# Kernel tuning notes

Hardware: AMD Instinct MI355X
Metric: run time of the kernel (lower is better)

Reference implementation:

```python
import jax, jax.numpy as jnp
import numpy as np

B, CIN, H, W = 8, 1, 192, 192
COUT, KH, KW = 8, 7, 7


def setup_inputs() -> dict:
    key = jax.random.key(0)
    k1, k2, k3 = jax.random.split(key, 3)
    x = jax.random.normal(k1, (B, CIN, H, W), dtype=jnp.float32)
    # original init: filter ~ N(0, 0.01), alpha = 0 (use small nonzero alpha)
    filt = 0.01 * jax.random.normal(k2, (COUT, CIN, KH, KW), dtype=jnp.float32)
    alpha = 0.1 * jax.random.normal(k3, (COUT, CIN), dtype=jnp.float32)
    return {"x": x, "filt": filt, "alpha": alpha}


def _smorph(x, filt, alpha):
    # x: [B, Cin, H, W]; filt: [Cout, Cin, kh, kw]; alpha: [Cout, Cin]
    b, cin, h, w = x.shape
    cout, _, kh, kw = filt.shape
    ho, wo = h - kh + 1, w - kw + 1  # 'valid' windowing as in _smorph_py
    # sliding-window patches: [B, Cin, kh*kw, Ho, Wo] (static slices, traced once)
    patches = jnp.stack(
        [x[:, :, ky:ky + ho, kx:kx + wo] for ky in range(kh) for kx in range(kw)],
        axis=2,
    )
    # s[b,co,ci,k,y,x] = input[b,ci,y+ky,x+kx] + filter[co,ci,ky,kx]
    s = patches[:, None] + filt.reshape(cout, cin, kh * kw, 1, 1)[None]
    a = alpha[None, :, :, None, None, None]  # broadcast over B, taps, space
    e = jnp.exp(a * s)
    num = jnp.sum(s * e, axis=(2, 3))  # sum over Cin and taps -> [B,Cout,Ho,Wo]
    den = jnp.sum(e, axis=(2, 3))
    return num / den


def reference(x, filt, alpha):
    # dual=False: single soft-morphology pass
    return _smorph(x, filt, alpha)
```

## Files before the change

### kernel.cpp

```cpp
#include <hip/hip_runtime.h>

#ifndef __has_builtin
#define __has_builtin(x) 0
#endif

__device__ __forceinline__ float fexp2(float v) {
#if __has_builtin(__builtin_amdgcn_exp2f)
    return __builtin_amdgcn_exp2f(v);
#else
    return exp2f(v);
#endif
}
__device__ __forceinline__ float frcp(float v) {
#if __has_builtin(__builtin_amdgcn_rcpf)
    return __builtin_amdgcn_rcpf(v);
#else
    return 1.0f / v;
#endif
}

constexpr int B_    = 8;
constexpr int H_    = 192;
constexpr int W_    = 192;
constexpr int COUT_ = 8;
constexpr int KH_   = 7;
constexpr int KW_   = 7;
constexpr int HO_   = H_ - KH_ + 1;
constexpr int WO_   = W_ - KW_ + 1;
constexpr float LOG2E = 1.44269504088896340736f;

constexpr int NTHR = 128;
constexpr int TX   = 32;
constexpr int TY   = 8;
constexpr int IX   = TX + KW_ - 1;
constexpr int IY   = TY + KH_ - 1;
constexpr int NPIX = IX * IY;
constexpr int NSLOT = (NPIX + NTHR - 1) / NTHR;

__global__ void smorph_setup(const float* __restrict__ filt,
                             const float* __restrict__ alpha,
                             float* __restrict__ ws) {
    int i = threadIdx.x;
    if (i < COUT_ * KH_) {
        int c = i / 7, ky = i - c * 7;
        float a2 = alpha[c] * LOG2E;
        float* t = ws + (c * 7 + ky) * 16;
#pragma unroll
        for (int kx = 0; kx < 7; ++kx) {
            float f = filt[(c * 7 + ky) * 7 + kx];
            float F = fexp2(a2 * f);
            t[kx]     = F;
            t[8 + kx] = F * f;
        }
        t[7] = 0.f; t[15] = 0.f;
    }
}

__global__ __launch_bounds__(NTHR, 8) void smorph_main(
    const float* __restrict__ x,
    const float* __restrict__ alpha,
    const float* __restrict__ fg,
    float* __restrict__ out)
{
    __shared__ __align__(16) float2 PH[IY * IX];

    const int tx  = threadIdx.x;
    const int ty  = threadIdx.y;
    const int tid = ty * 32 + tx;
    const int bx0 = blockIdx.x * TX;
    const int by0 = blockIdx.y * TY;
    const int z   = blockIdx.z;
    const int c   = z & 7;
    const float* xb = x + (z >> 3) * (H_ * W_);
    const float a2  = alpha[c] * LOG2E;

#pragma unroll
    for (int s = 0; s < NSLOT; ++s) {
        const int i = tid + NTHR * s;
        if (i < NPIX) {
            const int iy = i / IX, ix = i - iy * IX;
            const float xv = xb[min(by0 + iy, H_ - 1) * W_ + min(bx0 + ix, W_ - 1)];
            const float P = fexp2(a2 * xv);
            PH[i] = make_float2(P, xv * P);
        }
    }
    __syncthreads();

    const int xs = tx & 15;
    const int yr = (ty << 1) | (tx >> 4);
    const int ox = bx0 + 2 * xs;
    const int oy = by0 + yr;
    const bool vx = (ox + 1 < WO_);

    float num0 = 0.f, den0 = 0.f, num1 = 0.f, den1 = 0.f;
    const float* tc = fg + c * (7 * 16);
#pragma unroll
    for (int ky = 0; ky < KH_; ++ky) {
        const float* t = tc + ky * 16;
        const float4* rp = (const float4*)&PH[(yr + ky) * IX + 2 * xs];
        float4 q0 = rp[0], q1 = rp[1], q2 = rp[2], q3 = rp[3];
        float P[8]  = {q0.x, q0.z, q1.x, q1.z, q2.x, q2.z, q3.x, q3.z};
        float Hh[8] = {q0.y, q0.w, q1.y, q1.w, q2.y, q2.w, q3.y, q3.w};
#pragma unroll
        for (int kx = 0; kx < 7; ++kx) {
            const float F = t[kx], G = t[8 + kx];
            num0 = fmaf(F, Hh[kx],     num0);
            num0 = fmaf(G, P[kx],      num0);
            den0 = fmaf(F, P[kx],      den0);
            num1 = fmaf(F, Hh[kx + 1], num1);
            num1 = fmaf(G, P[kx + 1],  num1);
            den1 = fmaf(F, P[kx + 1],  den1);
        }
    }

    if (vx && oy < HO_) {
        float2 o;
        o.x = num0 * frcp(den0);
        o.y = num1 * frcp(den1);
        *(float2*)&out[(z * HO_ + oy) * WO_ + ox] = o;
    }
}

extern "C" void kernel_launch(void* const* d_in, const int* in_sizes, int n_in,
                              void* d_out, int out_size, void* d_ws, size_t ws_size,
                              hipStream_t stream) {
    const float* x     = (const float*)d_in[0];
    const float* filt  = (const float*)d_in[1];
    const float* alpha = (const float*)d_in[2];
    float* out = (float*)d_out;
    float* ws  = (float*)d_ws;

    smorph_setup<<<1, 64, 0, stream>>>(filt, alpha, ws);

    dim3 block(32, 4, 1);
    dim3 grid((WO_ + TX - 1) / TX, (HO_ + TY - 1) / TY, B_ * COUT_);
    smorph_main<<<grid, block, 0, stream>>>(x, alpha, ws, out);
}
```

Before: 76.06 us.

## Drop shared-memory tile, load input rows directly and compute exp per thread

Removes the LDS staging tile and barrier; each thread now reads its input rows straight from global memory with vector loads and computes four adjacent outputs. Exponentials of the input are recomputed per thread per row instead of once per block-shared pixel, greatly increasing transcendental work. Launch shape becomes 1D 128 threads with 32x16 output tiles.

Result: slower. 227.0 us (+198.4%).

```diff
diff --git a/kernel.cpp b/kernel.cpp
--- a/kernel.cpp
+++ b/kernel.cpp
@@ -29,13 +29,10 @@
 constexpr int WO_   = W_ - KW_ + 1;
 constexpr float LOG2E = 1.44269504088896340736f;
 
-constexpr int NTHR = 128;
-constexpr int TX   = 32;
-constexpr int TY   = 8;
-constexpr int IX   = TX + KW_ - 1;
-constexpr int IY   = TY + KH_ - 1;
-constexpr int NPIX = IX * IY;
-constexpr int NSLOT = (NPIX + NTHR - 1) / NTHR;
+constexpr int XS_  = 8;
+constexpr int YR_  = 16;
+constexpr int TX   = 4 * XS_;
+constexpr int TY   = YR_;
 
 __global__ void smorph_setup(const float* __restrict__ filt,
                              const float* __restrict__ alpha,
@@ -56,69 +53,63 @@
     }
 }
 
-__global__ __launch_bounds__(NTHR, 8) void smorph_main(
+__global__ __launch_bounds__(128, 8) void smorph_main(
     const float* __restrict__ x,
     const float* __restrict__ alpha,
     const float* __restrict__ fg,
     float* __restrict__ out)
 {
-    __shared__ __align__(16) float2 PH[IY * IX];
+    const int tid = threadIdx.x;
+    const int xs  = tid & (XS_ - 1);
+    const int yr  = tid >> 3;
+    const int ox0 = blockIdx.x * TX + 4 * xs;
+    const int oy  = blockIdx.y * TY + yr;
+    if (oy >= HO_ || ox0 + 1 >= WO_) return;
 
-    const int tx  = threadIdx.x;
-    const int ty  = threadIdx.y;
-    const int tid = ty * 32 + tx;
-    const int bx0 = blockIdx.x * TX;
-    const int by0 = blockIdx.y * TY;
-    const int z   = blockIdx.z;
-    const int c   = z & 7;
+    const int z = blockIdx.z;
+    const int c = z & 7;
     const float* xb = x + (z >> 3) * (H_ * W_);
     const float a2  = alpha[c] * LOG2E;
+    const float* tc = fg + c * (7 * 16);
 
-#pragma unroll
-    for (int s = 0; s < NSLOT; ++s) {
-        const int i = tid + NTHR * s;
-        if (i < NPIX) {
-            const int iy = i / IX, ix = i - iy * IX;
-            const float xv = xb[min(by0 + iy, H_ - 1) * W_ + min(bx0 + ix, W_ - 1)];
-            const float P = fexp2(a2 * xv);
-            PH[i] = make_float2(P, xv * P);
-        }
-    }
-    __syncthreads();
+    const bool haveC  = (ox0 + 9) < W_;
+    const bool haveHi = (ox0 + 3) < WO_;
 
-    const int xs = tx & 15;
-    const int yr = (ty << 1) | (tx >> 4);
-    const int ox = bx0 + 2 * xs;
-    const int oy = by0 + yr;
-    const bool vx = (ox + 1 < WO_);
+    float num[4] = {0.f, 0.f, 0.f, 0.f};
+    float den[4] = {0.f, 0.f, 0.f, 0.f};
 
-    float num0 = 0.f, den0 = 0.f, num1 = 0.f, den1 = 0.f;
-    const float* tc = fg + c * (7 * 16);
 #pragma unroll
     for (int ky = 0; ky < KH_; ++ky) {
         const float* t = tc + ky * 16;
-        const float4* rp = (const float4*)&PH[(yr + ky) * IX + 2 * xs];
-        float4 q0 = rp[0], q1 = rp[1], q2 = rp[2], q3 = rp[3];
-        float P[8]  = {q0.x, q0.z, q1.x, q1.z, q2.x, q2.z, q3.x, q3.z};
-        float Hh[8] = {q0.y, q0.w, q1.y, q1.w, q2.y, q2.w, q3.y, q3.w};
+        const float* rb = xb + (oy + ky) * W_ + ox0;
+        const float4 a4 = *(const float4*)rb;
+        const float4 b4 = *(const float4*)(rb + 4);
+        const float2 c2 = haveC ? *(const float2*)(rb + 8) : make_float2(0.f, 0.f);
+        const float xr[10] = {a4.x, a4.y, a4.z, a4.w,
+                              b4.x, b4.y, b4.z, b4.w,
+                              c2.x, c2.y};
+        float P[10], Hh[10];
 #pragma unroll
-        for (int kx = 0; kx < 7; ++kx) {
+        for (int j = 0; j < 10; ++j) {
+            P[j]  = fexp2(a2 * xr[j]);
+            Hh[j] = xr[j] * P[j];
+        }
+#pragma unroll
+        for (int kx = 0; kx < KW_; ++kx) {
             const float F = t[kx], G = t[8 + kx];
-            num0 = fmaf(F, Hh[kx],     num0);
-            num0 = fmaf(G, P[kx],      num0);
-            den0 = fmaf(F, P[kx],      den0);
-            num1 = fmaf(F, Hh[kx + 1], num1);
-            num1 = fmaf(G, P[kx + 1],  num1);
-            den1 = fmaf(F, P[kx + 1],  den1);
+#pragma unroll
+            for (int o = 0; o < 4; ++o) {
+                num[o] = fmaf(F, Hh[kx + o], num[o]);
+                num[o] = fmaf(G, P[kx + o],  num[o]);
+                den[o] = fmaf(F, P[kx + o],  den[o]);
+            }
         }
     }
 
-    if (vx && oy < HO_) {
-        float2 o;
-        o.x = num0 * frcp(den0);
-        o.y = num1 * frcp(den1);
-        *(float2*)&out[(z * HO_ + oy) * WO_ + ox] = o;
-    }
+    float* ob = out + (size_t)(z * HO_ + oy) * WO_ + ox0;
+    *(float2*)ob = make_float2(num[0] * frcp(den[0]), num[1] * frcp(den[1]));
+    if (haveHi)
+        *(float2*)(ob + 2) = make_float2(num[2] * frcp(den[2]), num[3] * frcp(den[3]));
 }
 
 extern "C" void kernel_launch(void* const* d_in, const int* in_sizes, int n_in,
@@ -132,7 +123,7 @@
 
     smorph_setup<<<1, 64, 0, stream>>>(filt, alpha, ws);
 
-    dim3 block(32, 4, 1);
+    dim3 block(128, 1, 1);
     dim3 grid((WO_ + TX - 1) / TX, (HO_ + TY - 1) / TY, B_ * COUT_);
     smorph_main<<<grid, block, 0, stream>>>(x, alpha, ws, out);
 }
```
